# Kernel tuning notes

Measured on AMD Instinct MI355X. Metric: run time of the kernel, lower is better.

Reference implementation:

```python
import jax, jax.numpy as jnp
import numpy as np

B, L, C = 16, 2048, 256
H, R = 6, 32
HEAD_SCALE = 1.0 / np.sqrt(R)


def setup_inputs() -> dict:
    key = jax.random.key(0)
    k1, k2, k3, k4 = jax.random.split(key, 4)
    feats = jax.random.normal(k1, (B, L + 1, C), dtype=jnp.float32)
    Wq = jax.random.normal(k2, (H * R, C), dtype=jnp.float32) * (1.0 / np.sqrt(C))
    Wk = jax.random.normal(k3, (H * R, C), dtype=jnp.float32) * (1.0 / np.sqrt(C))
    Wd = jax.random.normal(k4, (1, C), dtype=jnp.float32) * (1.0 / np.sqrt(C))
    bd = jnp.zeros((1,), dtype=jnp.float32)
    logit_scale = jnp.ones((), dtype=jnp.float32)
    return {"feats": feats, "Wq": Wq, "Wk": Wk, "Wd": Wd, "bd": bd,
            "logit_scale": logit_scale}


def _fold_vertices(feats):
    # drop leading token, pair-average: [B, L+1, C] -> [B, L//2, C]
    x = feats[:, 1:]
    b, l, c = x.shape
    return x.reshape(b, l // 2, 2, c).mean(axis=2)


def reference(feats, Wq, Wk, Wd, bd, logit_scale):
    x = _fold_vertices(feats)                     # [B, N, C]
    b, n, _ = x.shape
    Q = (x @ Wq.T).reshape(b, n, H, R)            # [B, N, H, R]
    K = (x @ Wk.T).reshape(b, n, H, R)
    # sum over heads of per-head low-rank QK^T == contraction over folded (H*R)
    S = jnp.einsum('bnhr,bmhr->bnm', Q, K) * HEAD_SCALE   # [B, N, N]
    d = (x @ Wd.T + bd).squeeze(-1)               # [B, N]
    idx = jnp.arange(n)
    S = S.at[:, idx, idx].add(d)
    return S * jnp.maximum(logit_scale, 0.01)
```

## Files before the change

### kernel.cpp

```cpp
#include <hip/hip_runtime.h>
#include <stdint.h>


#define HD_SCALE 0.17677669529663687f

typedef __bf16 bf16_t;
typedef bf16_t bf16x8 __attribute__((ext_vector_type(8)));
typedef float f32x4 __attribute__((ext_vector_type(4)));
typedef unsigned short ushort8_t __attribute__((ext_vector_type(8)));

__device__ __forceinline__ unsigned short f2bf(float f) {
  unsigned int u = __float_as_uint(f);
  return (unsigned short)((u + 0x7fffu + ((u >> 16) & 1u)) >> 16);
}

__device__ __forceinline__ void gload16(const void* g, void* l) {
  __builtin_amdgcn_global_load_lds(
      (const __attribute__((address_space(1))) void*)g,
      (__attribute__((address_space(3))) void*)l, 16, 0, 0);
}

__global__ __launch_bounds__(256) void k_pack(const float* __restrict__ Wq,
                                              const float* __restrict__ Wk,
                                              unsigned short* __restrict__ Wt) {
  const int flat = blockIdx.x * 256 + threadIdx.x;
  const int kc = flat / 384;
  const int row = flat - kc * 384;
  const float* src =
      (row < 192) ? (Wq + (size_t)row * 256) : (Wk + (size_t)(row - 192) * 256);
  const float4 a = *(const float4*)(src + kc * 8);
  const float4 b = *(const float4*)(src + kc * 8 + 4);
  ushort8_t v;
  v[0] = f2bf(a.x); v[1] = f2bf(a.y); v[2] = f2bf(a.z); v[3] = f2bf(a.w);
  v[4] = f2bf(b.x); v[5] = f2bf(b.y); v[6] = f2bf(b.z); v[7] = f2bf(b.w);
  *(ushort8_t*)(Wt + (size_t)flat * 8) = v;
}

__global__ __launch_bounds__(512) void k_fproj(const float* __restrict__ feats,
                                               const float* __restrict__ Wd,
                                               const float* __restrict__ bd,
                                               const unsigned short* __restrict__ Wt,
                                               float* __restrict__ dvec,
                                               unsigned short* __restrict__ QK) {
  __shared__ unsigned short As[64 * 256];
  const int t = threadIdx.x;
  const int m0 = blockIdx.x * 64;

  {
    const int row = t >> 3;
    const int gr = m0 + row;
    const int b = gr >> 10, n = gr & 1023;
    const float* r0 = feats + ((size_t)b * 2049 + 1 + 2 * n) * 256;
    float dot = 0.f;
#pragma unroll
    for (int q = 0; q < 4; ++q) {
      const int kc = (t & 7) + q * 8;
      const float4 p0a = *(const float4*)(r0 + kc * 8);
      const float4 p0b = *(const float4*)(r0 + kc * 8 + 4);
      const float4 p1a = *(const float4*)(r0 + 256 + kc * 8);
      const float4 p1b = *(const float4*)(r0 + 256 + kc * 8 + 4);
      const float4 wa = *(const float4*)(Wd + kc * 8);
      const float4 wb = *(const float4*)(Wd + kc * 8 + 4);
      const float x0 = (p0a.x + p1a.x) * 0.5f, x1 = (p0a.y + p1a.y) * 0.5f;
      const float x2 = (p0a.z + p1a.z) * 0.5f, x3 = (p0a.w + p1a.w) * 0.5f;
      const float x4 = (p0b.x + p1b.x) * 0.5f, x5 = (p0b.y + p1b.y) * 0.5f;
      const float x6 = (p0b.z + p1b.z) * 0.5f, x7 = (p0b.w + p1b.w) * 0.5f;
      dot += x0 * wa.x + x1 * wa.y + x2 * wa.z + x3 * wa.w +
             x4 * wb.x + x5 * wb.y + x6 * wb.z + x7 * wb.w;
      ushort8_t v;
      v[0] = f2bf(x0); v[1] = f2bf(x1); v[2] = f2bf(x2); v[3] = f2bf(x3);
      v[4] = f2bf(x4); v[5] = f2bf(x5); v[6] = f2bf(x6); v[7] = f2bf(x7);
      const int pos = kc ^ (row & 7);
      *(ushort8_t*)&As[(row * 32 + pos) * 8] = v;
    }
    dot += __shfl_down(dot, 4, 64);
    dot += __shfl_down(dot, 2, 64);
    dot += __shfl_down(dot, 1, 64);
    if ((t & 7) == 0) dvec[gr] = dot + bd[0];
  }
  __syncthreads();

  const int w = t >> 6, l = t & 63;
  const int wr = w >> 2, wc = w & 3;
  const int quad = l >> 4, lr = l & 15;

  f32x4 acc[2][6] = {};
#pragma unroll
  for (int kk = 0; kk < 4; ++kk) {
#pragma unroll
    for (int s = 0; s < 2; ++s) {
      const int kc = kk * 8 + s * 4 + quad;
      bf16x8 a[2], bb[6];
#pragma unroll
      for (int i = 0; i < 2; ++i) {
        const int row = wr * 32 + i * 16 + lr;
        const int pos = kc ^ (row & 7);
        a[i] = *(const bf16x8*)&As[(row * 32 + pos) * 8];
      }
#pragma unroll
      for (int j = 0; j < 6; ++j) {
        const int row = wc * 96 + j * 16 + lr;
        bb[j] = *(const bf16x8*)(Wt + ((size_t)kc * 384 + row) * 8);
      }
#pragma unroll
      for (int i = 0; i < 2; ++i)
#pragma unroll
        for (int j = 0; j < 6; ++j)
          acc[i][j] = __builtin_amdgcn_mfma_f32_16x16x32_bf16(a[i], bb[j],
                                                              acc[i][j], 0, 0, 0);
    }
  }

#pragma unroll
  for (int i = 0; i < 2; ++i)
#pragma unroll
    for (int j = 0; j < 6; ++j)
#pragma unroll
      for (int r = 0; r < 4; ++r) {
        const int rowq = m0 + wr * 32 + i * 16 + quad * 4 + r;
        const int col = wc * 96 + j * 16 + lr;
        QK[(size_t)rowq * 384 + col] = f2bf(acc[i][j][r]);
      }
}

__global__ __launch_bounds__(256) void k_score(const unsigned short* __restrict__ QK,
                                               const float* __restrict__ dvec,
                                               const float* __restrict__ logit_scale,
                                               float* __restrict__ out) {
  __shared__ unsigned short As[128 * 64];
  __shared__ unsigned short Bs[128 * 64];
  const int t = threadIdx.x;
  const int w = t >> 6, l = t & 63;

  const int flat = blockIdx.x + (blockIdx.y << 3) + (blockIdx.z << 6);
  const int xcd = flat & 7, j0 = flat >> 3;
  const int b = (xcd << 1) | (j0 >> 6);
  const int jj = j0 & 63;
  const int mt = jj & 7, nt = jj >> 3;

  const int m0 = mt * 128;
  const int n0 = nt * 128;
  const int wm = w >> 1, wn = w & 1;
  const int quad = l >> 4, lr = l & 15;
  const size_t qbase = (size_t)b * 1024 * 384;

  f32x4 acc[4][4] = {};

  for (int kk = 0; kk < 3; ++kk) {
    const int k0 = kk * 64;
    __syncthreads();
#pragma unroll
    for (int i = 0; i < 4; ++i) {
      const int e = i * 256 + t;
      const int row = e >> 3;
      const int kc = (e & 7) ^ (row & 7);
      gload16(QK + qbase + (size_t)(n0 + row) * 384 + k0 + kc * 8,
              &As[(i * 256 + (w << 6)) * 8]);
      gload16(QK + qbase + (size_t)(m0 + row) * 384 + 192 + k0 + kc * 8,
              &Bs[(i * 256 + (w << 6)) * 8]);
    }
    __syncthreads();

#pragma unroll
    for (int s = 0; s < 2; ++s) {
      bf16x8 a[4], bb[4];
#pragma unroll
      for (int i = 0; i < 4; ++i) {
        const int row = wm * 64 + i * 16 + lr;
        const int pos = (s * 4 + quad) ^ (row & 7);
        a[i] = *(const bf16x8*)&As[row * 64 + pos * 8];
      }
#pragma unroll
      for (int j = 0; j < 4; ++j) {
        const int row = wn * 64 + j * 16 + lr;
        const int pos = (s * 4 + quad) ^ (row & 7);
        bb[j] = *(const bf16x8*)&Bs[row * 64 + pos * 8];
      }
#pragma unroll
      for (int i = 0; i < 4; ++i)
#pragma unroll
        for (int j = 0; j < 4; ++j)
          acc[i][j] = __builtin_amdgcn_mfma_f32_16x16x32_bf16(a[i], bb[j],
                                                              acc[i][j], 0, 0, 0);
    }
  }

  const float ls = fmaxf(logit_scale[0], 0.01f);
  const bool diag_block = (m0 == n0);
#pragma unroll
  for (int i = 0; i < 4; ++i)
#pragma unroll
    for (int j = 0; j < 4; ++j)
#pragma unroll
      for (int r = 0; r < 4; ++r) {
        const int nr = n0 + wm * 64 + i * 16 + quad * 4 + r;
        const int mc = m0 + wn * 64 + j * 16 + lr;
        float v = acc[i][j][r] * HD_SCALE;
        if (diag_block && nr == mc) v += dvec[b * 1024 + nr];
        __builtin_nontemporal_store(v * ls,
            &out[((size_t)b << 20) + (size_t)nr * 1024 + mc]);
      }
}

extern "C" void kernel_launch(void* const* d_in, const int* in_sizes, int n_in,
                              void* d_out, int out_size, void* d_ws, size_t ws_size,
                              hipStream_t stream) {
  const float* feats = (const float*)d_in[0];
  const float* Wq = (const float*)d_in[1];
  const float* Wk = (const float*)d_in[2];
  const float* Wd = (const float*)d_in[3];
  const float* bd = (const float*)d_in[4];
  const float* ls = (const float*)d_in[5];
  float* out = (float*)d_out;

  uint8_t* ws = (uint8_t*)d_ws;
  unsigned short* QK = (unsigned short*)ws;
  float* dvec = (float*)(ws + (12u << 20));
  unsigned short* Wt = (unsigned short*)(ws + (12u << 20) + (64u << 10));

  hipLaunchKernelGGL(k_pack, dim3(48), dim3(256), 0, stream, Wq, Wk, Wt);
  hipLaunchKernelGGL(k_fproj, dim3(256), dim3(512), 0, stream, feats, Wd, bd, Wt,
                     dvec, QK);
  hipLaunchKernelGGL(k_score, dim3(8, 8, 16), dim3(256), 0, stream, QK, dvec, ls, out);
}
```

Before: 123.5 us.

## Store Q/K in k-chunk-major layout and load MFMA operands directly from global

The projection kernel now writes Q/K in a k-chunk-major layout ([batch][chunk of 8][row][8]) and runs with 32-row blocks of 256 threads. The score kernel drops its LDS staging and barriers and reads MFMA fragments straight from global memory, where each lane's 16-byte load is contiguous and coalesced across rows. It also sets launch bounds to allow 3 blocks per CU. This removes LDS traffic and synchronisation in exchange for relying on L1/L2 for operand reuse, so each fragment is fetched from cache by several waves.

```diff
diff --git a/kernel.cpp b/kernel.cpp
--- a/kernel.cpp
+++ b/kernel.cpp
@@ -12,12 +12,6 @@
 __device__ __forceinline__ unsigned short f2bf(float f) {
   unsigned int u = __float_as_uint(f);
   return (unsigned short)((u + 0x7fffu + ((u >> 16) & 1u)) >> 16);
-}
-
-__device__ __forceinline__ void gload16(const void* g, void* l) {
-  __builtin_amdgcn_global_load_lds(
-      (const __attribute__((address_space(1))) void*)g,
-      (__attribute__((address_space(3))) void*)l, 16, 0, 0);
 }
 
 __global__ __launch_bounds__(256) void k_pack(const float* __restrict__ Wq,
@@ -36,21 +30,23 @@
   *(ushort8_t*)(Wt + (size_t)flat * 8) = v;
 }
 
-__global__ __launch_bounds__(512) void k_fproj(const float* __restrict__ feats,
+__global__ __launch_bounds__(256) void k_fproj(const float* __restrict__ feats,
                                                const float* __restrict__ Wd,
                                                const float* __restrict__ bd,
                                                const unsigned short* __restrict__ Wt,
                                                float* __restrict__ dvec,
-                                               unsigned short* __restrict__ QK) {
-  __shared__ unsigned short As[64 * 256];
+                                               unsigned short* __restrict__ QKt) {
+  __shared__ unsigned short As[32 * 256];
   const int t = threadIdx.x;
-  const int m0 = blockIdx.x * 64;
+  const int m0 = blockIdx.x * 32;
+  const int bq = m0 >> 10;
+  const size_t qkbase = (size_t)bq * 48 * 1024 * 8;
 
   {
     const int row = t >> 3;
     const int gr = m0 + row;
-    const int b = gr >> 10, n = gr & 1023;
-    const float* r0 = feats + ((size_t)b * 2049 + 1 + 2 * n) * 256;
+    const int n = gr & 1023;
+    const float* r0 = feats + ((size_t)bq * 2049 + 1 + 2 * n) * 256;
     float dot = 0.f;
 #pragma unroll
     for (int q = 0; q < 4; ++q) {
@@ -81,7 +77,6 @@
   __syncthreads();
 
   const int w = t >> 6, l = t & 63;
-  const int wr = w >> 2, wc = w & 3;
   const int quad = l >> 4, lr = l & 15;
 
   f32x4 acc[2][6] = {};
@@ -93,13 +88,13 @@
       bf16x8 a[2], bb[6];
 #pragma unroll
       for (int i = 0; i < 2; ++i) {
-        const int row = wr * 32 + i * 16 + lr;
+        const int row = i * 16 + lr;
         const int pos = kc ^ (row & 7);
         a[i] = *(const bf16x8*)&As[(row * 32 + pos) * 8];
       }
 #pragma unroll
       for (int j = 0; j < 6; ++j) {
-        const int row = wc * 96 + j * 16 + lr;
+        const int row = w * 96 + j * 16 + lr;
         bb[j] = *(const bf16x8*)(Wt + ((size_t)kc * 384 + row) * 8);
       }
 #pragma unroll
@@ -117,18 +112,18 @@
     for (int j = 0; j < 6; ++j)
 #pragma unroll
       for (int r = 0; r < 4; ++r) {
-        const int rowq = m0 + wr * 32 + i * 16 + quad * 4 + r;
-        const int col = wc * 96 + j * 16 + lr;
-        QK[(size_t)rowq * 384 + col] = f2bf(acc[i][j][r]);
-      }
-}
-
-__global__ __launch_bounds__(256) void k_score(const unsigned short* __restrict__ QK,
-                                               const float* __restrict__ dvec,
-                                               const float* __restrict__ logit_scale,
-                                               float* __restrict__ out) {
-  __shared__ unsigned short As[128 * 64];
-  __shared__ unsigned short Bs[128 * 64];
+        const int nloc = (m0 & 1023) + i * 16 + quad * 4 + r;
+        const int col = w * 96 + j * 16 + lr;
+        QKt[qkbase + ((size_t)(col >> 3) * 1024 + nloc) * 8 + (col & 7)] =
+            f2bf(acc[i][j][r]);
+      }
+}
+
+__global__ __launch_bounds__(256, 3) void k_score(
+    const unsigned short* __restrict__ QKt,
+    const float* __restrict__ dvec,
+    const float* __restrict__ logit_scale,
+    float* __restrict__ out) {
   const int t = threadIdx.x;
   const int w = t >> 6, l = t & 63;
 
@@ -142,39 +137,26 @@
   const int n0 = nt * 128;
   const int wm = w >> 1, wn = w & 1;
   const int quad = l >> 4, lr = l & 15;
-  const size_t qbase = (size_t)b * 1024 * 384;
+  const unsigned short* Qb = QKt + (size_t)b * 48 * 1024 * 8;
 
   f32x4 acc[4][4] = {};
 
+#pragma unroll
   for (int kk = 0; kk < 3; ++kk) {
-    const int k0 = kk * 64;
-    __syncthreads();
-#pragma unroll
-    for (int i = 0; i < 4; ++i) {
-      const int e = i * 256 + t;
-      const int row = e >> 3;
-      const int kc = (e & 7) ^ (row & 7);
-      gload16(QK + qbase + (size_t)(n0 + row) * 384 + k0 + kc * 8,
-              &As[(i * 256 + (w << 6)) * 8]);
-      gload16(QK + qbase + (size_t)(m0 + row) * 384 + 192 + k0 + kc * 8,
-              &Bs[(i * 256 + (w << 6)) * 8]);
-    }
-    __syncthreads();
-
 #pragma unroll
     for (int s = 0; s < 2; ++s) {
+      const int kcq = kk * 8 + s * 4 + quad;
+      const int kck = 24 + kcq;
       bf16x8 a[4], bb[4];
 #pragma unroll
       for (int i = 0; i < 4; ++i) {
-        const int row = wm * 64 + i * 16 + lr;
-        const int pos = (s * 4 + quad) ^ (row & 7);
-        a[i] = *(const bf16x8*)&As[row * 64 + pos * 8];
+        const int row = n0 + wm * 64 + i * 16 + lr;
+        a[i] = *(const bf16x8*)(Qb + ((size_t)kcq * 1024 + row) * 8);
       }
 #pragma unroll
       for (int j = 0; j < 4; ++j) {
-        const int row = wn * 64 + j * 16 + lr;
-        const int pos = (s * 4 + quad) ^ (row & 7);
-        bb[j] = *(const bf16x8*)&Bs[row * 64 + pos * 8];
+        const int row = m0 + wn * 64 + j * 16 + lr;
+        bb[j] = *(const bf16x8*)(Qb + ((size_t)kck * 1024 + row) * 8);
       }
 #pragma unroll
       for (int i = 0; i < 4; ++i)
@@ -214,12 +196,12 @@
   float* out = (float*)d_out;
 
   uint8_t* ws = (uint8_t*)d_ws;
-  unsigned short* QK = (unsigned short*)ws;
+  unsigned short* QKt = (unsigned short*)ws;
   float* dvec = (float*)(ws + (12u << 20));
   unsigned short* Wt = (unsigned short*)(ws + (12u << 20) + (64u << 10));
 
   hipLaunchKernelGGL(k_pack, dim3(48), dim3(256), 0, stream, Wq, Wk, Wt);
-  hipLaunchKernelGGL(k_fproj, dim3(256), dim3(512), 0, stream, feats, Wd, bd, Wt,
-                     dvec, QK);
-  hipLaunchKernelGGL(k_score, dim3(8, 8, 16), dim3(256), 0, stream, QK, dvec, ls, out);
-}
+  hipLaunchKernelGGL(k_fproj, dim3(512), dim3(256), 0, stream, feats, Wd, bd, Wt,
+                     dvec, QKt);
+  hipLaunchKernelGGL(k_score, dim3(8, 8, 16), dim3(256), 0, stream, QKt, dvec, ls, out);
+}
```

Result: slower. 128.0 us (+3.6%).

## Double-buffer LDS tiles in score kernel to overlap loads with MFMA

Applied to the files above, without the earlier changes.

The score kernel now uses two LDS buffers per operand and issues the second K-chunk's global-to-LDS loads before computing the first. Partial vmcnt waits with explicit barriers let the third chunk's loads overlap compute on the second. This targets the load latency exposed by the former load-sync-compute loop, at the cost of doubling LDS use to 64KB, which may lower occupancy. It also relies on hand-counted vmcnt values being correct.

```diff
diff --git a/kernel.cpp b/kernel.cpp
--- a/kernel.cpp
+++ b/kernel.cpp
@@ -127,8 +127,8 @@
                                                const float* __restrict__ dvec,
                                                const float* __restrict__ logit_scale,
                                                float* __restrict__ out) {
-  __shared__ unsigned short As[128 * 64];
-  __shared__ unsigned short Bs[128 * 64];
+  __shared__ unsigned short As[2][128 * 64];
+  __shared__ unsigned short Bs[2][128 * 64];
   const int t = threadIdx.x;
   const int w = t >> 6, l = t & 63;
 
@@ -146,21 +146,20 @@
 
   f32x4 acc[4][4] = {};
 
-  for (int kk = 0; kk < 3; ++kk) {
-    const int k0 = kk * 64;
-    __syncthreads();
+  auto stage = [&](int buf, int k0) {
 #pragma unroll
     for (int i = 0; i < 4; ++i) {
       const int e = i * 256 + t;
       const int row = e >> 3;
       const int kc = (e & 7) ^ (row & 7);
       gload16(QK + qbase + (size_t)(n0 + row) * 384 + k0 + kc * 8,
-              &As[(i * 256 + (w << 6)) * 8]);
+              &As[buf][(i * 256 + (w << 6)) * 8]);
       gload16(QK + qbase + (size_t)(m0 + row) * 384 + 192 + k0 + kc * 8,
-              &Bs[(i * 256 + (w << 6)) * 8]);
-    }
-    __syncthreads();
-
+              &Bs[buf][(i * 256 + (w << 6)) * 8]);
+    }
+  };
+
+  auto compute = [&](int buf) {
 #pragma unroll
     for (int s = 0; s < 2; ++s) {
       bf16x8 a[4], bb[4];
@@ -168,13 +167,13 @@
       for (int i = 0; i < 4; ++i) {
         const int row = wm * 64 + i * 16 + lr;
         const int pos = (s * 4 + quad) ^ (row & 7);
-        a[i] = *(const bf16x8*)&As[row * 64 + pos * 8];
+        a[i] = *(const bf16x8*)&As[buf][row * 64 + pos * 8];
       }
 #pragma unroll
       for (int j = 0; j < 4; ++j) {
         const int row = wn * 64 + j * 16 + lr;
         const int pos = (s * 4 + quad) ^ (row & 7);
-        bb[j] = *(const bf16x8*)&Bs[row * 64 + pos * 8];
+        bb[j] = *(const bf16x8*)&Bs[buf][row * 64 + pos * 8];
       }
 #pragma unroll
       for (int i = 0; i < 4; ++i)
@@ -183,7 +182,25 @@
           acc[i][j] = __builtin_amdgcn_mfma_f32_16x16x32_bf16(a[i], bb[j],
                                                               acc[i][j], 0, 0, 0);
     }
-  }
+  };
+
+  stage(0, 0);
+  stage(1, 64);
+  asm volatile("s_waitcnt vmcnt(8)" ::: "memory");
+  __builtin_amdgcn_s_barrier();
+  __builtin_amdgcn_sched_barrier(0);
+  compute(0);
+  __builtin_amdgcn_s_barrier();
+  __builtin_amdgcn_sched_barrier(0);
+  stage(0, 128);
+  asm volatile("s_waitcnt vmcnt(8)" ::: "memory");
+  __builtin_amdgcn_s_barrier();
+  __builtin_amdgcn_sched_barrier(0);
+  compute(1);
+  asm volatile("s_waitcnt vmcnt(0)" ::: "memory");
+  __builtin_amdgcn_s_barrier();
+  __builtin_amdgcn_sched_barrier(0);
+  compute(0);
 
   const float ls = fmaxf(logit_scale[0], 0.01f);
   const bool diag_block = (m0 == n0);
```

New measurement: 125.1 us. No clear change (+1.2%).
